# Kernel optimization log

Hardware: AMD Instinct MI355X
Metric: run time of the kernel (lower is better)

The kernel has to match this reference:

```python
import jax, jax.numpy as jnp
import numpy as np

ALPHA = 20.0
GAMMA = 4.0
GN_GROUPS = 32
EPS = 1e-5
DIRS = ['lr', 'rl', 'tb', 'bt']


def _propagate(seq, gate, Wi, bi, Ws, bs, pb, reverse):
    # seq: [N, C, L], gate: [N, 1, L]
    if reverse:
        seq = seq[..., ::-1]
        gate = gate[..., ::-1]
    proj = jnp.einsum('ncl,dc->ndl', seq, Wi) + bi[None, :, None]  # input_proj (k=1 conv)
    proj_t = jnp.moveaxis(proj, -1, 0)   # [L, N, C]
    gate_t = jnp.moveaxis(gate, -1, 0)   # [L, N, 1]
    const = bs + pb                       # state_proj bias + extra bias

    def step(prev, inp):
        p, g = inp
        cur = p + (prev * g) @ Ws.T + const
        nxt = jax.nn.relu(cur)
        return nxt, nxt

    init = jnp.zeros(seq.shape[:2], seq.dtype)  # [N, C]
    _, out = jax.lax.scan(step, init, (proj_t, gate_t))
    out = jnp.moveaxis(out, 0, -1)  # [N, C, L]
    if reverse:
        out = out[..., ::-1]
    return out


def _group_norm(x, w, b):
    B, C, H, W = x.shape
    g = GN_GROUPS
    xg = x.reshape(B, g, C // g, H, W)
    mu = xg.mean(axis=(2, 3, 4), keepdims=True)
    var = xg.var(axis=(2, 3, 4), keepdims=True)
    xn = ((xg - mu) * jax.lax.rsqrt(var + EPS)).reshape(B, C, H, W)
    return xn * w[None, :, None, None] + b[None, :, None, None]


def setup_inputs() -> dict:
    key = jax.random.key(0)
    ks = jax.random.split(key, 6)
    B, C, H, W = 8, 256, 128, 128
    s = 1.0 / np.sqrt(C)
    return {
        'feature': jax.random.normal(ks[0], (B, C, H, W), jnp.float32),
        'boundary_logits': jax.random.normal(ks[1], (B, 1, H, W), jnp.float32),
        'beta': jnp.ones((1,), jnp.float32),
        'W_in': jax.random.normal(ks[2], (4, C, C), jnp.float32) * s,
        'b_in': jnp.zeros((4, C), jnp.float32),
        'W_s': jax.random.normal(ks[3], (4, C, C), jnp.float32) * s,
        'b_s': jnp.zeros((4, C), jnp.float32),
        'p_bias': jnp.zeros((4, C), jnp.float32),
        'out_w': jax.random.normal(ks[4], (C, C), jnp.float32) * s,
        'out_b': jnp.zeros((C,), jnp.float32),
        'gn_w': jnp.ones((C,), jnp.float32),
        'gn_b': jnp.zeros((C,), jnp.float32),
    }


def reference(feature, boundary_logits, beta, W_in, b_in, W_s, b_s, p_bias, out_w, out_b, gn_w, gn_b):
    B, C, H, W = feature.shape
    # gate: p = clamp(1 - beta * sigmoid(alpha * sigmoid(b) - gamma), 0, 1)
    conf = jnp.clip(1.0 - beta[0] * jax.nn.sigmoid(ALPHA * jax.nn.sigmoid(boundary_logits) - GAMMA), 0.0, 1.0)

    # horizontal sequences: [B*H, C, W]
    seq_h = feature.transpose(0, 2, 1, 3).reshape(B * H, C, W)
    gate_h = conf.transpose(0, 2, 1, 3).reshape(B * H, 1, W)
    # vertical sequences: [B*W, C, H]
    seq_v = feature.transpose(0, 3, 1, 2).reshape(B * W, C, H)
    gate_v = conf.transpose(0, 3, 1, 2).reshape(B * W, 1, H)

    outs = []
    for i, d in enumerate(DIRS):
        if d in ('lr', 'rl'):
            o = _propagate(seq_h, gate_h, W_in[i], b_in[i], W_s[i], b_s[i], p_bias[i], d == 'rl')
            o = o.reshape(B, H, C, W).transpose(0, 2, 1, 3)
        else:
            o = _propagate(seq_v, gate_v, W_in[i], b_in[i], W_s[i], b_s[i], p_bias[i], d == 'bt')
            o = o.reshape(B, W, C, H).transpose(0, 2, 3, 1)
        outs.append(o)

    fused = outs[0] + outs[1] + outs[2] + outs[3]
    fused = jnp.einsum('bchw,dc->bdhw', fused, out_w) + out_b[None, :, None, None]
    fused = fused + feature  # residual
    return _group_norm(fused, gn_w, gn_b)
```

## Files before the change

### kernel.cpp

```cpp
#include <hip/hip_runtime.h>
#include <hip/hip_bf16.h>

#define BB 8
#define CC 256
#define HH 128
#define WW 128
#define HW (HH*WW)
#define NPIX (BB*HW)

__global__ __launch_bounds__(256) void k_conf(const float* __restrict__ bl,
                                              const float* __restrict__ beta,
                                              float* __restrict__ conf,
                                              float* __restrict__ stats) {
  const int t = threadIdx.x;
  if (blockIdx.x == 0) { stats[t] = 0.f; stats[t + 256] = 0.f; }
  const int i = blockIdx.x * 256 + t;
  float x = bl[i];
  float s1 = 1.f / (1.f + expf(-x));
  float s2 = 1.f / (1.f + expf(-(20.f * s1 - 4.f)));
  float cv = 1.f - beta[0] * s2;
  conf[i] = fminf(fmaxf(cv, 0.f), 1.f);
}

__global__ __launch_bounds__(256) void k_tr(const float* __restrict__ W_in,
                                            const float* __restrict__ out_w,
                                            float* __restrict__ wT) {
  const int i = blockIdx.x * 256 + threadIdx.x;
  const int m = i >> 16;
  const int rr = i & 65535;
  const int c = rr >> 8;
  const int d = rr & 255;
  const float* src = (m < 4) ? (W_in + m * 65536) : out_w;
  wT[i] = src[d * 256 + c];
}

__global__ __launch_bounds__(256) void k_proj_gemm(const float* __restrict__ feature,
                                                   const float* __restrict__ wT,
                                                   const float* __restrict__ bias,
                                                   float* __restrict__ proj,
                                                   int vertical) {
  __shared__ float Xs[64 * 256];
  const int t = threadIdx.x;
  const int b = blockIdx.y;
  const int p0 = blockIdx.x * 64;

  {
    const int j = t & 63, c0 = t >> 6;
#pragma unroll
    for (int cc = 0; cc < 64; ++cc) {
      int c = cc * 4 + c0;
      Xs[c * 64 + j] = feature[((b * CC + c) << 14) + p0 + j];
    }
  }
  __syncthreads();

  const int d = t;
  float acc[64];
#pragma unroll
  for (int i = 0; i < 64; ++i) acc[i] = 0.f;

#pragma unroll 4
  for (int c = 0; c < 256; ++c) {
    float w = wT[c * 256 + d];
#pragma unroll
    for (int p4 = 0; p4 < 16; ++p4) {
      float4 xv = *reinterpret_cast<const float4*>(&Xs[c * 64 + p4 * 4]);
      acc[p4 * 4 + 0] += w * xv.x;
      acc[p4 * 4 + 1] += w * xv.y;
      acc[p4 * 4 + 2] += w * xv.z;
      acc[p4 * 4 + 3] += w * xv.w;
    }
  }

  const float bia = bias[d];
#pragma unroll
  for (int jj = 0; jj < 64; ++jj) {
    int p = p0 + jj;
    int pos = vertical ? (((p & 127) << 7) + (p >> 7)) : p;
    proj[(b * HW + pos) * 256 + d] = acc[jj] + bia;
  }
}

__global__ __launch_bounds__(512, 2) void k_scan(const float* __restrict__ proj,
                                                 const float* __restrict__ conf,
                                                 const float* __restrict__ Ws,
                                                 const float* __restrict__ b_s,
                                                 const float* __restrict__ p_bias,
                                                 float* __restrict__ accum,
                                                 int vertical, int rev, int first) {
  __shared__ __align__(16) float hbuf[2][4][CC];
  const int t = threadIdx.x;
  const int g = t & 7;
  const int rbg = t >> 3;
  const int s0 = blockIdx.x * 4;

  float4 W4[4][8];
#pragma unroll
  for (int i = 0; i < 4; ++i) {
    const float* wrow = Ws + (rbg * 4 + i) * CC + g * 32;
#pragma unroll
    for (int j = 0; j < 8; ++j) {
      const int cj = (j + g) & 7;
      W4[i][j] = *reinterpret_cast<const float4*>(wrow + cj * 4);
    }
  }
  const float4 bs4 = *reinterpret_cast<const float4*>(b_s + rbg * 4);
  const float4 pb4 = *reinterpret_cast<const float4*>(p_bias + rbg * 4);
  float4 cst4 = make_float4(bs4.x + pb4.x, bs4.y + pb4.y, bs4.z + pb4.z, bs4.w + pb4.w);

  {
    float* hb0 = &hbuf[0][0][0];
    hb0[t] = 0.f;
    hb0[t + 512] = 0.f;
  }

  const int dp = rev ? -CC : CC;
  const int dc = vertical ? (rev ? -WW : WW) : (rev ? -1 : 1);
  const int da = vertical ? (rev ? -(WW * CC) : (WW * CC)) : dp;
  const int pstart = rev ? 127 : 0;

  int pix = 0, cix = 0, aix = 0;
  if (g < 4) {
    int n = s0 + g;
    if (!vertical) {
      pix = (n * WW + pstart) * CC + rbg * 4;
      cix = n * WW + pstart;
      aix = pix;
    } else {
      int b = n >> 7, wc = n & 127;
      pix = (n * HH + pstart) * CC + rbg * 4;
      cix = b * HW + pstart * WW + wc;
      aix = (b * HW + pstart * WW + wc) * CC + rbg * 4;
    }
  }

  float4 pj = make_float4(0.f, 0.f, 0.f, 0.f), pjn = pj, ard = pj, arn = pj;
  float gg = 0.f, ggn = 0.f;
  if (g < 4) {
    pj = *reinterpret_cast<const float4*>(proj + pix);
    gg = conf[cix];
    if (!first) ard = *reinterpret_cast<const float4*>(accum + aix);
    pix += dp; cix += dc;
  }
  __syncthreads();

  for (int k = 0; k < 128; ++k) {
    if (g < 4) {
      if (k < 127) {
        pjn = *reinterpret_cast<const float4*>(proj + pix);
        ggn = conf[cix];
        if (!first) arn = *reinterpret_cast<const float4*>(accum + aix + da);
      }
    }

    float dt[4][4];
#pragma unroll
    for (int s = 0; s < 4; ++s)
#pragma unroll
      for (int i = 0; i < 4; ++i) dt[s][i] = 0.f;

    const float* hb = &hbuf[k & 1][0][0];
#pragma unroll
    for (int j = 0; j < 8; ++j) {
      const int off = g * 32 + (((j + g) & 7) << 2);
#pragma unroll
      for (int s = 0; s < 4; ++s) {
        float4 hv = *reinterpret_cast<const float4*>(hb + s * CC + off);
#pragma unroll
        for (int i = 0; i < 4; ++i) {
          dt[s][i] += W4[i][j].x * hv.x + W4[i][j].y * hv.y +
                      W4[i][j].z * hv.z + W4[i][j].w * hv.w;
        }
      }
    }

#pragma unroll
    for (int s = 0; s < 4; ++s)
#pragma unroll
      for (int i = 0; i < 4; ++i) {
        float v = dt[s][i];
        v += __shfl_xor(v, 1);
        v += __shfl_xor(v, 2);
        v += __shfl_xor(v, 4);
        dt[s][i] = v;
      }

    if (g < 4) {
      float d0 = (g == 0) ? dt[0][0] : (g == 1) ? dt[1][0] : (g == 2) ? dt[2][0] : dt[3][0];
      float d1 = (g == 0) ? dt[0][1] : (g == 1) ? dt[1][1] : (g == 2) ? dt[2][1] : dt[3][1];
      float d2 = (g == 0) ? dt[0][2] : (g == 1) ? dt[1][2] : (g == 2) ? dt[2][2] : dt[3][2];
      float d3 = (g == 0) ? dt[0][3] : (g == 1) ? dt[1][3] : (g == 2) ? dt[2][3] : dt[3][3];
      float4 hn;
      hn.x = fmaxf(pj.x + gg * d0 + cst4.x, 0.f);
      hn.y = fmaxf(pj.y + gg * d1 + cst4.y, 0.f);
      hn.z = fmaxf(pj.z + gg * d2 + cst4.z, 0.f);
      hn.w = fmaxf(pj.w + gg * d3 + cst4.w, 0.f);
      *reinterpret_cast<float4*>(&hbuf[(k + 1) & 1][g][rbg * 4]) = hn;
      float4 av;
      if (first) av = hn;
      else av = make_float4(hn.x + ard.x, hn.y + ard.y, hn.z + ard.z, hn.w + ard.w);
      *reinterpret_cast<float4*>(accum + aix) = av;
      aix += da;
      pj = pjn; gg = ggn; ard = arn;
      pix += dp; cix += dc;
    }
    __syncthreads();
  }
}

__global__ __launch_bounds__(256) void k_out_gemm(const float* __restrict__ fused,
                                                  const float* __restrict__ owT,
                                                  const float* __restrict__ out_b,
                                                  const float* __restrict__ feature,
                                                  float* __restrict__ out,
                                                  float* __restrict__ stats) {
  __shared__ float Fs[64 * 256];
  const int t = threadIdx.x;
  const int b = blockIdx.y;
  const int p0 = blockIdx.x * 64;

  {
    const int px = t >> 2, cq = t & 3;
    const float* src = fused + ((b * HW + p0 + px) * 256 + cq * 64);
#pragma unroll
    for (int kk = 0; kk < 16; ++kk) {
      float4 v = *reinterpret_cast<const float4*>(src + kk * 4);
      int c = cq * 64 + kk * 4;
      Fs[(c + 0) * 64 + px] = v.x; Fs[(c + 1) * 64 + px] = v.y;
      Fs[(c + 2) * 64 + px] = v.z; Fs[(c + 3) * 64 + px] = v.w;
    }
  }
  __syncthreads();

  const int d = t;
  float acc[64];
#pragma unroll
  for (int i = 0; i < 64; ++i) acc[i] = 0.f;

#pragma unroll 4
  for (int c = 0; c < 256; ++c) {
    float w = owT[c * 256 + d];
#pragma unroll
    for (int p4 = 0; p4 < 16; ++p4) {
      float4 xv = *reinterpret_cast<const float4*>(&Fs[c * 64 + p4 * 4]);
      acc[p4 * 4 + 0] += w * xv.x;
      acc[p4 * 4 + 1] += w * xv.y;
      acc[p4 * 4 + 2] += w * xv.z;
      acc[p4 * 4 + 3] += w * xv.w;
    }
  }

  const float bia = out_b[d];
  const int obase = ((b * 256 + d) << 14) + p0;
  const float* fsrc = feature + obase;
  float s1 = 0.f, s2 = 0.f;
#pragma unroll
  for (int j = 0; j < 64; ++j) {
    float z = acc[j] + bia + fsrc[j];
    out[obase + j] = z;
    s1 += z; s2 += z * z;
  }
  s1 += __shfl_xor(s1, 1); s2 += __shfl_xor(s2, 1);
  s1 += __shfl_xor(s1, 2); s2 += __shfl_xor(s2, 2);
  s1 += __shfl_xor(s1, 4); s2 += __shfl_xor(s2, 4);
  if ((d & 7) == 0) {
    int gidx = d >> 3;
    atomicAdd(&stats[(b * 32 + gidx) * 2 + 0], s1);
    atomicAdd(&stats[(b * 32 + gidx) * 2 + 1], s2);
  }
}

__global__ __launch_bounds__(256) void k_norm(float* __restrict__ out,
                                              const float* __restrict__ stats,
                                              const float* __restrict__ gn_w,
                                              const float* __restrict__ gn_b) {
  const int i = (blockIdx.x * 256 + threadIdx.x) << 2;
  const int c = (i >> 14) & 255;
  const int b = i >> 22;
  const int g = c >> 3;
  float s1 = stats[(b * 32 + g) * 2 + 0];
  float s2 = stats[(b * 32 + g) * 2 + 1];
  const float invN = 1.f / 131072.f;
  float mu = s1 * invN;
  float var = fmaxf(s2 * invN - mu * mu, 0.f);
  float is = rsqrtf(var + 1e-5f);
  float wmul = gn_w[c] * is;
  float badd = gn_b[c] - mu * wmul;
  float4 z = *reinterpret_cast<float4*>(&out[i]);
  z.x = z.x * wmul + badd; z.y = z.y * wmul + badd;
  z.z = z.z * wmul + badd; z.w = z.w * wmul + badd;
  *reinterpret_cast<float4*>(&out[i]) = z;
}

extern "C" void kernel_launch(void* const* d_in, const int* in_sizes, int n_in,
                              void* d_out, int out_size, void* d_ws, size_t ws_size,
                              hipStream_t stream) {
  const float* feature = (const float*)d_in[0];
  const float* blog    = (const float*)d_in[1];
  const float* beta    = (const float*)d_in[2];
  const float* W_in    = (const float*)d_in[3];
  const float* b_in    = (const float*)d_in[4];
  const float* W_s     = (const float*)d_in[5];
  const float* b_s     = (const float*)d_in[6];
  const float* p_bias  = (const float*)d_in[7];
  const float* out_w   = (const float*)d_in[8];
  const float* out_b   = (const float*)d_in[9];
  const float* gn_w    = (const float*)d_in[10];
  const float* gn_b    = (const float*)d_in[11];
  float* out = (float*)d_out;

  float* ws    = (float*)d_ws;
  float* proj  = ws;
  float* accum = ws + 33554432;
  float* conf  = ws + 67108864;
  float* stats = ws + 67239936;
  float* wT    = ws + 67240448;

  k_conf<<<NPIX / 256, 256, 0, stream>>>(blog, beta, conf, stats);
  k_tr<<<(5 * 65536) / 256, 256, 0, stream>>>(W_in, out_w, wT);

  for (int dir = 0; dir < 4; ++dir) {
    const int vertical = (dir >= 2);
    const int rev = (dir == 1 || dir == 3);
    k_proj_gemm<<<dim3(HW / 64, BB), 256, 0, stream>>>(
        feature, wT + dir * 65536, b_in + dir * 256, proj, vertical);
    k_scan<<<256, 512, 0, stream>>>(
        proj, conf, W_s + dir * 65536, b_s + dir * 256, p_bias + dir * 256,
        accum, vertical, rev, dir == 0);
  }

  k_out_gemm<<<dim3(HW / 64, BB), 256, 0, stream>>>(
      accum, wT + 4 * 65536, out_b, feature, out, stats);
  k_norm<<<(BB * CC * HW) / 1024, 256, 0, stream>>>(out, stats, gn_w, gn_b);
}
```

Before: 3.497 ms.

## Retile projection/output GEMMs and widen scan to 1024 threads with transpose-reduce

Both 1x1-conv GEMMs now use 2D register tiles (4 output channels x 16 pixels, or 16 channels x 4 pixels) with float4 weight loads and vectorised stores, replacing the one-channel-per-thread scheme. The intent is more reuse per shared-memory read and coalesced writes. The recurrent scan kernel now uses 1024 threads per block, so all threads do useful work instead of half sitting idle on the update step. It splits the dot product 16 ways and uses a butterfly transpose-reduce with shuffles, so each lane finishes with one output element. The trade-offs are fewer blocks per CU on the scan and different register pressure in the GEMMs.

```diff
diff --git a/kernel.cpp b/kernel.cpp
--- a/kernel.cpp
+++ b/kernel.cpp
@@ -39,7 +39,7 @@
                                                    const float* __restrict__ bias,
                                                    float* __restrict__ proj,
                                                    int vertical) {
-  __shared__ float Xs[64 * 256];
+  __shared__ float Xs[256 * 64];
   const int t = threadIdx.x;
   const int b = blockIdx.y;
   const int p0 = blockIdx.x * 64;
@@ -54,156 +54,155 @@
   }
   __syncthreads();
 
-  const int d = t;
-  float acc[64];
-#pragma unroll
-  for (int i = 0; i < 64; ++i) acc[i] = 0.f;
-
-#pragma unroll 4
+  const int q = t & 63;
+  const int p = t >> 6;
+
+  float acc[4][16];
+#pragma unroll
+  for (int ch = 0; ch < 4; ++ch)
+#pragma unroll
+    for (int px = 0; px < 16; ++px) acc[ch][px] = 0.f;
+
+#pragma unroll 2
   for (int c = 0; c < 256; ++c) {
-    float w = wT[c * 256 + d];
-#pragma unroll
-    for (int p4 = 0; p4 < 16; ++p4) {
-      float4 xv = *reinterpret_cast<const float4*>(&Xs[c * 64 + p4 * 4]);
-      acc[p4 * 4 + 0] += w * xv.x;
-      acc[p4 * 4 + 1] += w * xv.y;
-      acc[p4 * 4 + 2] += w * xv.z;
-      acc[p4 * 4 + 3] += w * xv.w;
-    }
-  }
-
-  const float bia = bias[d];
-#pragma unroll
-  for (int jj = 0; jj < 64; ++jj) {
-    int p = p0 + jj;
-    int pos = vertical ? (((p & 127) << 7) + (p >> 7)) : p;
-    proj[(b * HW + pos) * 256 + d] = acc[jj] + bia;
-  }
-}
-
-__global__ __launch_bounds__(512, 2) void k_scan(const float* __restrict__ proj,
-                                                 const float* __restrict__ conf,
-                                                 const float* __restrict__ Ws,
-                                                 const float* __restrict__ b_s,
-                                                 const float* __restrict__ p_bias,
-                                                 float* __restrict__ accum,
-                                                 int vertical, int rev, int first) {
+    const float4 w4 = *reinterpret_cast<const float4*>(wT + c * 256 + q * 4);
+#pragma unroll
+    for (int p4 = 0; p4 < 4; ++p4) {
+      const float4 xv = *reinterpret_cast<const float4*>(&Xs[c * 64 + p * 16 + p4 * 4]);
+      acc[0][p4 * 4 + 0] += w4.x * xv.x; acc[0][p4 * 4 + 1] += w4.x * xv.y;
+      acc[0][p4 * 4 + 2] += w4.x * xv.z; acc[0][p4 * 4 + 3] += w4.x * xv.w;
+      acc[1][p4 * 4 + 0] += w4.y * xv.x; acc[1][p4 * 4 + 1] += w4.y * xv.y;
+      acc[1][p4 * 4 + 2] += w4.y * xv.z; acc[1][p4 * 4 + 3] += w4.y * xv.w;
+      acc[2][p4 * 4 + 0] += w4.z * xv.x; acc[2][p4 * 4 + 1] += w4.z * xv.y;
+      acc[2][p4 * 4 + 2] += w4.z * xv.z; acc[2][p4 * 4 + 3] += w4.z * xv.w;
+      acc[3][p4 * 4 + 0] += w4.w * xv.x; acc[3][p4 * 4 + 1] += w4.w * xv.y;
+      acc[3][p4 * 4 + 2] += w4.w * xv.z; acc[3][p4 * 4 + 3] += w4.w * xv.w;
+    }
+  }
+
+  const float4 bia = *reinterpret_cast<const float4*>(bias + q * 4);
+#pragma unroll
+  for (int jj = 0; jj < 16; ++jj) {
+    const int pp = p0 + p * 16 + jj;
+    const int pos = vertical ? (((pp & 127) << 7) + (pp >> 7)) : pp;
+    float4 o = make_float4(acc[0][jj] + bia.x, acc[1][jj] + bia.y,
+                           acc[2][jj] + bia.z, acc[3][jj] + bia.w);
+    *reinterpret_cast<float4*>(&proj[(size_t)(b * HW + pos) * 256 + q * 4]) = o;
+  }
+}
+
+__global__ __launch_bounds__(1024) void k_scan(const float* __restrict__ proj,
+                                               const float* __restrict__ conf,
+                                               const float* __restrict__ Ws,
+                                               const float* __restrict__ b_s,
+                                               const float* __restrict__ p_bias,
+                                               float* __restrict__ accum,
+                                               int vertical, int rev, int first) {
   __shared__ __align__(16) float hbuf[2][4][CC];
   const int t = threadIdx.x;
-  const int g = t & 7;
-  const int rbg = t >> 3;
-  const int s0 = blockIdx.x * 4;
-
-  float4 W4[4][8];
+  const int g = t & 15;
+  const int rbg = t >> 4;
+  const int s_own = g >> 2;
+  const int row = rbg * 4 + (g & 3);
+
+  float4 W4[4][4];
 #pragma unroll
   for (int i = 0; i < 4; ++i) {
-    const float* wrow = Ws + (rbg * 4 + i) * CC + g * 32;
-#pragma unroll
-    for (int j = 0; j < 8; ++j) {
-      const int cj = (j + g) & 7;
-      W4[i][j] = *reinterpret_cast<const float4*>(wrow + cj * 4);
-    }
-  }
-  const float4 bs4 = *reinterpret_cast<const float4*>(b_s + rbg * 4);
-  const float4 pb4 = *reinterpret_cast<const float4*>(p_bias + rbg * 4);
-  float4 cst4 = make_float4(bs4.x + pb4.x, bs4.y + pb4.y, bs4.z + pb4.z, bs4.w + pb4.w);
-
-  {
-    float* hb0 = &hbuf[0][0][0];
-    hb0[t] = 0.f;
-    hb0[t + 512] = 0.f;
-  }
+    const float* wr = Ws + (rbg * 4 + i) * CC + g * 16;
+#pragma unroll
+    for (int j = 0; j < 4; ++j) {
+      const int cj = (j + (g >> 1)) & 3;
+      W4[i][j] = *reinterpret_cast<const float4*>(wr + cj * 4);
+    }
+  }
+  const float cst = b_s[row] + p_bias[row];
+
+  ((float*)hbuf)[t] = 0.f;
 
   const int dp = rev ? -CC : CC;
   const int dc = vertical ? (rev ? -WW : WW) : (rev ? -1 : 1);
   const int da = vertical ? (rev ? -(WW * CC) : (WW * CC)) : dp;
   const int pstart = rev ? 127 : 0;
 
-  int pix = 0, cix = 0, aix = 0;
-  if (g < 4) {
-    int n = s0 + g;
-    if (!vertical) {
-      pix = (n * WW + pstart) * CC + rbg * 4;
-      cix = n * WW + pstart;
-      aix = pix;
-    } else {
-      int b = n >> 7, wc = n & 127;
-      pix = (n * HH + pstart) * CC + rbg * 4;
-      cix = b * HW + pstart * WW + wc;
-      aix = (b * HW + pstart * WW + wc) * CC + rbg * 4;
-    }
-  }
-
-  float4 pj = make_float4(0.f, 0.f, 0.f, 0.f), pjn = pj, ard = pj, arn = pj;
-  float gg = 0.f, ggn = 0.f;
-  if (g < 4) {
-    pj = *reinterpret_cast<const float4*>(proj + pix);
-    gg = conf[cix];
-    if (!first) ard = *reinterpret_cast<const float4*>(accum + aix);
-    pix += dp; cix += dc;
-  }
+  const int n = blockIdx.x * 4 + s_own;
+  int pix, cix, aix;
+  if (!vertical) {
+    pix = (n * WW + pstart) * CC + row;
+    cix = n * WW + pstart;
+    aix = pix;
+  } else {
+    pix = (n * HH + pstart) * CC + row;
+    cix = (n >> 7) * HW + pstart * WW + (n & 127);
+    aix = ((n >> 7) * HW + pstart * WW + (n & 127)) * CC + row;
+  }
+
+  float pj = proj[pix];
+  float gg = conf[cix];
+  float ard = first ? 0.f : accum[aix];
+  pix += dp; cix += dc;
   __syncthreads();
 
   for (int k = 0; k < 128; ++k) {
-    if (g < 4) {
-      if (k < 127) {
-        pjn = *reinterpret_cast<const float4*>(proj + pix);
-        ggn = conf[cix];
-        if (!first) arn = *reinterpret_cast<const float4*>(accum + aix + da);
-      }
-    }
-
-    float dt[4][4];
-#pragma unroll
-    for (int s = 0; s < 4; ++s)
-#pragma unroll
-      for (int i = 0; i < 4; ++i) dt[s][i] = 0.f;
+    float pjn = 0.f, ggn = 0.f, arn = 0.f;
+    if (k < 127) {
+      pjn = proj[pix];
+      ggn = conf[cix];
+      if (!first) arn = accum[aix + da];
+    }
+
+    float dt[16];
+#pragma unroll
+    for (int v = 0; v < 16; ++v) dt[v] = 0.f;
 
     const float* hb = &hbuf[k & 1][0][0];
 #pragma unroll
-    for (int j = 0; j < 8; ++j) {
-      const int off = g * 32 + (((j + g) & 7) << 2);
+    for (int j = 0; j < 4; ++j) {
+      const int off = g * 16 + (((j + (g >> 1)) & 3) << 2);
 #pragma unroll
       for (int s = 0; s < 4; ++s) {
-        float4 hv = *reinterpret_cast<const float4*>(hb + s * CC + off);
+        const float4 hv = *reinterpret_cast<const float4*>(hb + s * CC + off);
 #pragma unroll
         for (int i = 0; i < 4; ++i) {
-          dt[s][i] += W4[i][j].x * hv.x + W4[i][j].y * hv.y +
-                      W4[i][j].z * hv.z + W4[i][j].w * hv.w;
+          dt[s * 4 + i] += W4[i][j].x * hv.x + W4[i][j].y * hv.y +
+                           W4[i][j].z * hv.z + W4[i][j].w * hv.w;
         }
       }
     }
 
 #pragma unroll
-    for (int s = 0; s < 4; ++s)
-#pragma unroll
-      for (int i = 0; i < 4; ++i) {
-        float v = dt[s][i];
-        v += __shfl_xor(v, 1);
-        v += __shfl_xor(v, 2);
-        v += __shfl_xor(v, 4);
-        dt[s][i] = v;
-      }
-
-    if (g < 4) {
-      float d0 = (g == 0) ? dt[0][0] : (g == 1) ? dt[1][0] : (g == 2) ? dt[2][0] : dt[3][0];
-      float d1 = (g == 0) ? dt[0][1] : (g == 1) ? dt[1][1] : (g == 2) ? dt[2][1] : dt[3][1];
-      float d2 = (g == 0) ? dt[0][2] : (g == 1) ? dt[1][2] : (g == 2) ? dt[2][2] : dt[3][2];
-      float d3 = (g == 0) ? dt[0][3] : (g == 1) ? dt[1][3] : (g == 2) ? dt[2][3] : dt[3][3];
-      float4 hn;
-      hn.x = fmaxf(pj.x + gg * d0 + cst4.x, 0.f);
-      hn.y = fmaxf(pj.y + gg * d1 + cst4.y, 0.f);
-      hn.z = fmaxf(pj.z + gg * d2 + cst4.z, 0.f);
-      hn.w = fmaxf(pj.w + gg * d3 + cst4.w, 0.f);
-      *reinterpret_cast<float4*>(&hbuf[(k + 1) & 1][g][rbg * 4]) = hn;
-      float4 av;
-      if (first) av = hn;
-      else av = make_float4(hn.x + ard.x, hn.y + ard.y, hn.z + ard.z, hn.w + ard.w);
-      *reinterpret_cast<float4*>(accum + aix) = av;
-      aix += da;
-      pj = pjn; gg = ggn; ard = arn;
-      pix += dp; cix += dc;
-    }
+    for (int jj = 0; jj < 8; ++jj) {
+      float send = (g & 8) ? dt[jj] : dt[jj + 8];
+      float recv = __shfl_xor(send, 8);
+      float keep = (g & 8) ? dt[jj + 8] : dt[jj];
+      dt[jj] = keep + recv;
+    }
+#pragma unroll
+    for (int jj = 0; jj < 4; ++jj) {
+      float send = (g & 4) ? dt[jj] : dt[jj + 4];
+      float recv = __shfl_xor(send, 4);
+      float keep = (g & 4) ? dt[jj + 4] : dt[jj];
+      dt[jj] = keep + recv;
+    }
+#pragma unroll
+    for (int jj = 0; jj < 2; ++jj) {
+      float send = (g & 2) ? dt[jj] : dt[jj + 2];
+      float recv = __shfl_xor(send, 2);
+      float keep = (g & 2) ? dt[jj + 2] : dt[jj];
+      dt[jj] = keep + recv;
+    }
+    {
+      float send = (g & 1) ? dt[0] : dt[1];
+      float recv = __shfl_xor(send, 1);
+      float keep = (g & 1) ? dt[1] : dt[0];
+      dt[0] = keep + recv;
+    }
+
+    const float hn = fmaxf(pj + gg * dt[0] + cst, 0.f);
+    hbuf[(k + 1) & 1][s_own][row] = hn;
+    accum[aix] = first ? hn : (hn + ard);
+    aix += da;
+    pj = pjn; gg = ggn; ard = arn;
+    pix += dp; cix += dc;
     __syncthreads();
   }
 }
@@ -214,14 +213,14 @@
                                                   const float* __restrict__ feature,
                                                   float* __restrict__ out,
                                                   float* __restrict__ stats) {
-  __shared__ float Fs[64 * 256];
+  __shared__ float Fs[256 * 64];
   const int t = threadIdx.x;
   const int b = blockIdx.y;
   const int p0 = blockIdx.x * 64;
 
   {
     const int px = t >> 2, cq = t & 3;
-    const float* src = fused + ((b * HW + p0 + px) * 256 + cq * 64);
+    const float* src = fused + ((size_t)(b * HW + p0 + px)) * 256 + cq * 64;
 #pragma unroll
     for (int kk = 0; kk < 16; ++kk) {
       float4 v = *reinterpret_cast<const float4*>(src + kk * 4);
@@ -232,41 +231,56 @@
   }
   __syncthreads();
 
-  const int d = t;
-  float acc[64];
-#pragma unroll
-  for (int i = 0; i < 64; ++i) acc[i] = 0.f;
-
-#pragma unroll 4
+  const int pq = t & 15;
+  const int cg = t >> 4;
+
+  float acc[16][4];
+#pragma unroll
+  for (int ch = 0; ch < 16; ++ch)
+#pragma unroll
+    for (int px = 0; px < 4; ++px) acc[ch][px] = 0.f;
+
+#pragma unroll 2
   for (int c = 0; c < 256; ++c) {
-    float w = owT[c * 256 + d];
-#pragma unroll
-    for (int p4 = 0; p4 < 16; ++p4) {
-      float4 xv = *reinterpret_cast<const float4*>(&Fs[c * 64 + p4 * 4]);
-      acc[p4 * 4 + 0] += w * xv.x;
-      acc[p4 * 4 + 1] += w * xv.y;
-      acc[p4 * 4 + 2] += w * xv.z;
-      acc[p4 * 4 + 3] += w * xv.w;
-    }
-  }
-
-  const float bia = out_b[d];
-  const int obase = ((b * 256 + d) << 14) + p0;
-  const float* fsrc = feature + obase;
-  float s1 = 0.f, s2 = 0.f;
-#pragma unroll
-  for (int j = 0; j < 64; ++j) {
-    float z = acc[j] + bia + fsrc[j];
-    out[obase + j] = z;
-    s1 += z; s2 += z * z;
-  }
-  s1 += __shfl_xor(s1, 1); s2 += __shfl_xor(s2, 1);
-  s1 += __shfl_xor(s1, 2); s2 += __shfl_xor(s2, 2);
-  s1 += __shfl_xor(s1, 4); s2 += __shfl_xor(s2, 4);
-  if ((d & 7) == 0) {
-    int gidx = d >> 3;
-    atomicAdd(&stats[(b * 32 + gidx) * 2 + 0], s1);
-    atomicAdd(&stats[(b * 32 + gidx) * 2 + 1], s2);
+    const float4 xv = *reinterpret_cast<const float4*>(&Fs[c * 64 + pq * 4]);
+#pragma unroll
+    for (int wi = 0; wi < 4; ++wi) {
+      const float4 w4 = *reinterpret_cast<const float4*>(owT + c * 256 + cg * 16 + wi * 4);
+      acc[wi * 4 + 0][0] += w4.x * xv.x; acc[wi * 4 + 0][1] += w4.x * xv.y;
+      acc[wi * 4 + 0][2] += w4.x * xv.z; acc[wi * 4 + 0][3] += w4.x * xv.w;
+      acc[wi * 4 + 1][0] += w4.y * xv.x; acc[wi * 4 + 1][1] += w4.y * xv.y;
+      acc[wi * 4 + 1][2] += w4.y * xv.z; acc[wi * 4 + 1][3] += w4.y * xv.w;
+      acc[wi * 4 + 2][0] += w4.z * xv.x; acc[wi * 4 + 2][1] += w4.z * xv.y;
+      acc[wi * 4 + 2][2] += w4.z * xv.z; acc[wi * 4 + 2][3] += w4.z * xv.w;
+      acc[wi * 4 + 3][0] += w4.w * xv.x; acc[wi * 4 + 3][1] += w4.w * xv.y;
+      acc[wi * 4 + 3][2] += w4.w * xv.z; acc[wi * 4 + 3][3] += w4.w * xv.w;
+    }
+  }
+
+  float s1a = 0.f, s2a = 0.f, s1b = 0.f, s2b = 0.f;
+#pragma unroll
+  for (int ch = 0; ch < 16; ++ch) {
+    const int cabs = cg * 16 + ch;
+    const float bia = out_b[cabs];
+    const size_t base = ((size_t)(b * 256 + cabs) << 14) + p0 + pq * 4;
+    const float4 f = *reinterpret_cast<const float4*>(feature + base);
+    float4 z = make_float4(acc[ch][0] + bia + f.x, acc[ch][1] + bia + f.y,
+                           acc[ch][2] + bia + f.z, acc[ch][3] + bia + f.w);
+    *reinterpret_cast<float4*>(&out[base]) = z;
+    float ps = z.x + z.y + z.z + z.w;
+    float pq2 = z.x * z.x + z.y * z.y + z.z * z.z + z.w * z.w;
+    if (ch < 8) { s1a += ps; s2a += pq2; } else { s1b += ps; s2b += pq2; }
+  }
+#pragma unroll
+  for (int m = 1; m <= 8; m <<= 1) {
+    s1a += __shfl_xor(s1a, m); s2a += __shfl_xor(s2a, m);
+    s1b += __shfl_xor(s1b, m); s2b += __shfl_xor(s2b, m);
+  }
+  if (pq == 0) {
+    atomicAdd(&stats[(b * 32 + cg * 2 + 0) * 2 + 0], s1a);
+    atomicAdd(&stats[(b * 32 + cg * 2 + 0) * 2 + 1], s2a);
+    atomicAdd(&stats[(b * 32 + cg * 2 + 1) * 2 + 0], s1b);
+    atomicAdd(&stats[(b * 32 + cg * 2 + 1) * 2 + 1], s2b);
   }
 }
 
@@ -324,7 +338,7 @@
     const int rev = (dir == 1 || dir == 3);
     k_proj_gemm<<<dim3(HW / 64, BB), 256, 0, stream>>>(
         feature, wT + dir * 65536, b_in + dir * 256, proj, vertical);
-    k_scan<<<256, 512, 0, stream>>>(
+    k_scan<<<256, 1024, 0, stream>>>(
         proj, conf, W_s + dir * 65536, b_s + dir * 256, p_bias + dir * 256,
         accum, vertical, rev, dir == 0);
   }
```

New measurement: 2.974 ms. -14.9%, faster.
